# Kernel tuning notes

Hardware: AMD Instinct MI355X
Metric: run time of the kernel (lower is better)

Reference implementation:

```python
import jax, jax.numpy as jnp
import numpy as np


def setup_inputs() -> dict:
    key = jax.random.key(0)
    x = jax.random.normal(key, (16, 2048, 512), dtype=jnp.float32)
    return {"x": x}


def reference(x):
    # Cosine (L2-normalized) self-attention.
    # norm: [B, N, 1] L2 norm over feature dim
    norm = jnp.sqrt(jnp.sum(x * x, axis=2, keepdims=True))
    # scores[b, i, j] = <x_i, x_j> / (|x_i| |x_j|)  -> [B, N, N]
    scores = jnp.einsum('bnd,bmd->bnm', x, x) / (norm * jnp.swapaxes(norm, -2, -1))
    p_attn = jax.nn.softmax(scores, axis=-1)
    # output: [B, N, D]
    return jnp.einsum('bnm,bmd->bnd', p_attn, x)
```

## Files before the change

kernel.cpp:

```cpp
#include <hip/hip_runtime.h>
#include <hip/hip_bf16.h>
#include <cstdint>
#include <cstddef>

#define BB 16
#define NN 2048
#define DD 512

typedef _Float16 f16x8 __attribute__((ext_vector_type(8)));
typedef _Float16 f16x4 __attribute__((ext_vector_type(4)));
typedef float f32x4 __attribute__((ext_vector_type(4)));
typedef unsigned int u32x4 __attribute__((ext_vector_type(4)));

__device__ __forceinline__ void async_ld16(void* lds, const void* g) {
    __builtin_amdgcn_global_load_lds(
        (const __attribute__((address_space(1))) unsigned int*)(uintptr_t)g,
        (__attribute__((address_space(3))) unsigned int*)(uint32_t)(uintptr_t)lds,
        16, 0, 0);
}

#define VM_WAIT(n) asm volatile("s_waitcnt vmcnt(" #n ")" ::: "memory")
#define RAW_BAR()  do { asm volatile("" ::: "memory"); __builtin_amdgcn_s_barrier(); asm volatile("" ::: "memory"); } while (0)
#define LGKM_BAR() do { asm volatile("s_waitcnt lgkmcnt(0)" ::: "memory"); \
                        __builtin_amdgcn_s_barrier();                      \
                        __builtin_amdgcn_sched_barrier(0); } while (0)

__global__ __launch_bounds__(256) void k_prep(const float* __restrict__ x,
                                              _Float16* __restrict__ xhn,
                                              _Float16* __restrict__ vT,
                                              float* __restrict__ denom) {
    __shared__ _Float16 t[512 * 66];
    const int tid = threadIdx.x, lane = tid & 63, w = tid >> 6;
    const int b = blockIdx.y, j0 = blockIdx.x * 64;
    if (tid < 64) denom[b * NN + j0 + tid] = 0.f;
    const float* xb = x + ((size_t)b * NN + j0) * DD;

    for (int rr = 0; rr < 16; ++rr) {
        const int jj = w * 16 + rr;
        const float* xr = xb + (size_t)jj * DD;
        f32x4 a = __builtin_nontemporal_load((const f32x4*)xr + lane);
        f32x4 c = __builtin_nontemporal_load((const f32x4*)xr + lane + 64);
        float ss = a[0]*a[0] + a[1]*a[1] + a[2]*a[2] + a[3]*a[3]
                 + c[0]*c[0] + c[1]*c[1] + c[2]*c[2] + c[3]*c[3];
        #pragma unroll
        for (int o = 1; o < 64; o <<= 1) ss += __shfl_xor(ss, o);
        const float rn = 1.0f / sqrtf(ss);
        _Float16* dst = xhn + ((size_t)b * NN + j0 + jj) * DD;
        f16x4 v0 = {(_Float16)(a[0]*rn), (_Float16)(a[1]*rn), (_Float16)(a[2]*rn), (_Float16)(a[3]*rn)};
        f16x4 v1 = {(_Float16)(c[0]*rn), (_Float16)(c[1]*rn), (_Float16)(c[2]*rn), (_Float16)(c[3]*rn)};
        *(f16x4*)(dst + 4 * lane) = v0;
        *(f16x4*)(dst + 256 + 4 * lane) = v1;
        const int d0 = 4 * lane, d1 = 256 + 4 * lane;
        t[(d0 + 0) * 66 + jj] = (_Float16)a[0];
        t[(d0 + 1) * 66 + jj] = (_Float16)a[1];
        t[(d0 + 2) * 66 + jj] = (_Float16)a[2];
        t[(d0 + 3) * 66 + jj] = (_Float16)a[3];
        t[(d1 + 0) * 66 + jj] = (_Float16)c[0];
        t[(d1 + 1) * 66 + jj] = (_Float16)c[1];
        t[(d1 + 2) * 66 + jj] = (_Float16)c[2];
        t[(d1 + 3) * 66 + jj] = (_Float16)c[3];
    }
    LGKM_BAR();
    #pragma unroll
    for (int it = 0; it < 16; ++it) {
        const int id = it * 256 + tid;
        const int d = id >> 3, ch = (id & 7) * 8;
        const uint32_t* tp = (const uint32_t*)&t[d * 66 + ch];
        uint4 v = {tp[0], tp[1], tp[2], tp[3]};
        *(uint4*)(vT + ((size_t)b * DD + d) * NN + j0 + ch) = v;
    }
}

__global__ __launch_bounds__(256, 4) void k_scores(const _Float16* __restrict__ xhn,
                                                   _Float16* __restrict__ W,
                                                   float* __restrict__ denom) {
    __shared__ _Float16 smem[17408];
    const int tid = threadIdx.x;
    const int lane = tid & 63, wv = tid >> 6;
    const int wr = wv >> 1, wc = wv & 1;
    const int m_ = lane & 15, quad = lane >> 4;
    const int b = blockIdx.z;

    const int swz = (blockIdx.x % 8) * 17 + blockIdx.x / 8;
    int rem = swz, ti = 0, rowlen = NN / 128;
    while (rem >= rowlen) { rem -= rowlen; ++ti; --rowlen; }
    const int tj = ti + rem;
    const int I = ti * 128, J = tj * 128;
    const bool diag = (ti == tj);

    const _Float16* Ab = xhn + ((size_t)b * NN + I) * DD;
    const _Float16* Bb = xhn + ((size_t)b * NN + J) * DD;

    f32x4 acc[4][4];
    #pragma unroll
    for (int i = 0; i < 4; ++i)
        #pragma unroll
        for (int j = 0; j < 4; ++j) acc[i][j] = (f32x4){0.f, 0.f, 0.f, 0.f};

    const int sub = lane >> 3;
    const int swc = (lane & 7) ^ sub;
    const _Float16* agl = Ab + (size_t)(wv * 32 + sub) * DD + swc * 8;
    const _Float16* bgl = Bb + (size_t)(wv * 32 + sub) * DD + swc * 8;
    _Float16* As = smem;
    _Float16* Bs = smem + 8192;

    for (int kb = 0; kb < DD / 64; ++kb) {
        const int k0 = kb * 64;
        #pragma unroll
        for (int c = 0; c < 4; ++c) {
            async_ld16(&As[(wv * 32 + c * 8) * 64], agl + (size_t)c * 8 * DD + k0);
            async_ld16(&Bs[(wv * 32 + c * 8) * 64], bgl + (size_t)c * 8 * DD + k0);
        }
        VM_WAIT(0);
        RAW_BAR();
        __builtin_amdgcn_s_setprio(1);
        #pragma unroll
        for (int kc = 0; kc < 2; ++kc) {
            f16x8 af[4], bf[4];
            #pragma unroll
            for (int t = 0; t < 4; ++t) {
                const int Ra = wr * 64 + t * 16 + m_;
                const int Rb = wc * 64 + t * 16 + m_;
                af[t] = *(const f16x8*)&As[Ra * 64 + (((kc * 4 + quad) ^ (Ra & 7)) * 8)];
                bf[t] = *(const f16x8*)&Bs[Rb * 64 + (((kc * 4 + quad) ^ (Rb & 7)) * 8)];
            }
            #pragma unroll
            for (int i = 0; i < 4; ++i)
                #pragma unroll
                for (int j = 0; j < 4; ++j)
                    acc[i][j] = __builtin_amdgcn_mfma_f32_16x16x32_f16(af[i], bf[j], acc[i][j], 0, 0, 0);
        }
        __builtin_amdgcn_s_setprio(0);
        RAW_BAR();
    }

    f16x4 wq[4][4];
    float rowpart[4][4];
    float colpart[4] = {0.f, 0.f, 0.f, 0.f};
    #pragma unroll
    for (int i = 0; i < 4; ++i)
        #pragma unroll
        for (int r = 0; r < 4; ++r) rowpart[i][r] = 0.f;

    #pragma unroll
    for (int i = 0; i < 4; ++i) {
        #pragma unroll
        for (int j = 0; j < 4; ++j) {
            #pragma unroll
            for (int r = 0; r < 4; ++r) {
                const float w = __expf(acc[i][j][r]);
                wq[i][j][r] = (_Float16)w;
                rowpart[i][r] += w;
                colpart[j] += w;
            }
        }
    }

    #pragma unroll
    for (int i = 0; i < 4; ++i) {
        #pragma unroll
        for (int r = 0; r < 4; ++r) {
            float s = rowpart[i][r];
            s += __shfl_xor(s, 1);
            s += __shfl_xor(s, 2);
            s += __shfl_xor(s, 4);
            s += __shfl_xor(s, 8);
            if (m_ == 0)
                atomicAdd(&denom[b * NN + I + wr * 64 + i * 16 + quad * 4 + r], s);
        }
    }
    if (!diag) {
        #pragma unroll
        for (int j = 0; j < 4; ++j) {
            float s = colpart[j];
            s += __shfl_xor(s, 16);
            s += __shfl_xor(s, 32);
            if (quad == 0)
                atomicAdd(&denom[b * NN + J + wc * 64 + j * 16 + m_], s);
        }
    }

    LGKM_BAR();

    _Float16* WtT = smem;
    #pragma unroll
    for (int i = 0; i < 4; ++i) {
        const int rowb = wr * 64 + i * 16 + quad * 4;
        #pragma unroll
        for (int j = 0; j < 4; ++j) {
            const int col = wc * 64 + j * 16 + m_;
            *(f16x4*)&WtT[col * 136 + rowb] = wq[i][j];
        }
    }
    LGKM_BAR();
    #pragma unroll
    for (int it2 = 0; it2 < 8; ++it2) {
        const int id = it2 * 256 + tid;
        const int rr = id >> 4, off = (id & 15) * 8;
        *(uint4*)(W + ((size_t)b * NN + J + rr) * NN + I + off) =
            *(const uint4*)&WtT[rr * 136 + off];
    }
    if (!diag) {
        LGKM_BAR();
        _Float16* Wt = smem;
        #pragma unroll
        for (int i = 0; i < 4; ++i) {
            const int rowb = wr * 64 + i * 16 + quad * 4;
            #pragma unroll
            for (int j = 0; j < 4; ++j) {
                const int col = wc * 64 + j * 16 + m_;
                #pragma unroll
                for (int r = 0; r < 4; ++r)
                    Wt[(rowb + r) * 136 + col] = wq[i][j][r];
            }
        }
        LGKM_BAR();
        #pragma unroll
        for (int it2 = 0; it2 < 8; ++it2) {
            const int id = it2 * 256 + tid;
            const int rr = id >> 4, off = (id & 15) * 8;
            *(uint4*)(W + ((size_t)b * NN + I + rr) * NN + J + off) =
                *(const uint4*)&Wt[rr * 136 + off];
        }
    }
}

__global__ __launch_bounds__(512, 4) void k_pv(const _Float16* __restrict__ W,
                                               const _Float16* __restrict__ vT,
                                               const float* __restrict__ denom,
                                               float* __restrict__ out) {
    __shared__ _Float16 smem[24576];
    __shared__ float rdI[128];
    const int tid = threadIdx.x;
    const int lane = tid & 63, w = tid >> 6;
    const int wr = w >> 2, wcol = w & 3;
    const int m_ = lane & 15, quad = lane >> 4;

    const int bx = blockIdx.x;
    const int xcd = bx & 7, slot = bx >> 3;
    const int b  = (slot >> 5) * 8 + xcd;
    const int s2 = slot & 31;
    const int I  = (s2 >> 1) * 128;
    const int D0 = (s2 & 1) * 256;

    const _Float16* Ab = W  + ((size_t)b * NN + I) * NN;
    const _Float16* Bb = vT + ((size_t)b * DD + D0) * NN;

    const int sub = lane >> 3;
    const int swc = (lane & 7) ^ sub;
    const _Float16* agl = Ab + (size_t)(w * 16 + sub) * NN + swc * 8;
    const _Float16* bgl = Bb + (size_t)(w * 32 + sub) * NN + swc * 8;
    _Float16* As = smem;
    _Float16* Bs = smem + 8192;

    f32x4 acc[4][4];
    #pragma unroll
    for (int i = 0; i < 4; ++i)
        #pragma unroll
        for (int j = 0; j < 4; ++j) acc[i][j] = (f32x4){0.f, 0.f, 0.f, 0.f};

    for (int kb = 0; kb < NN / 64; ++kb) {
        const int k0 = kb * 64;
        #pragma unroll
        for (int c = 0; c < 2; ++c)
            async_ld16(&As[(w * 16 + c * 8) * 64], agl + (size_t)c * 8 * NN + k0);
        #pragma unroll
        for (int c = 0; c < 4; ++c)
            async_ld16(&Bs[(w * 32 + c * 8) * 64], bgl + (size_t)c * 8 * NN + k0);
        VM_WAIT(0);
        RAW_BAR();
        __builtin_amdgcn_s_setprio(1);
        #pragma unroll
        for (int kc = 0; kc < 2; ++kc) {
            f16x8 af[4], bf[4];
            #pragma unroll
            for (int t = 0; t < 4; ++t) {
                const int Ra = wr * 64 + t * 16 + m_;
                const int Rb = wcol * 64 + t * 16 + m_;
                af[t] = *(const f16x8*)&As[Ra * 64 + (((kc * 4 + quad) ^ (Ra & 7)) * 8)];
                bf[t] = *(const f16x8*)&Bs[Rb * 64 + (((kc * 4 + quad) ^ (Rb & 7)) * 8)];
            }
            #pragma unroll
            for (int i = 0; i < 4; ++i)
                #pragma unroll
                for (int j = 0; j < 4; ++j)
                    acc[i][j] = __builtin_amdgcn_mfma_f32_16x16x32_f16(af[i], bf[j], acc[i][j], 0, 0, 0);
        }
        __builtin_amdgcn_s_setprio(0);
        RAW_BAR();
    }

    if (tid < 128) rdI[tid] = 1.0f / denom[b * NN + I + tid];
    LGKM_BAR();

    #pragma unroll
    for (int i = 0; i < 4; ++i) {
        const int rowb = wr * 64 + i * 16 + quad * 4;
        #pragma unroll
        for (int r = 0; r < 4; ++r) {
            const float sc = rdI[rowb + r];
            float* op = out + ((size_t)(b * NN + I + rowb + r)) * DD + D0;
            #pragma unroll
            for (int j = 0; j < 4; ++j)
                __builtin_nontemporal_store(acc[i][j][r] * sc,
                                            op + wcol * 64 + j * 16 + m_);
        }
    }
}

extern "C" void kernel_launch(void* const* d_in, const int* in_sizes, int n_in,
                              void* d_out, int out_size, void* d_ws, size_t ws_size,
                              hipStream_t stream) {
    const float* x = (const float*)d_in[0];
    char* ws = (char*)d_ws;
    _Float16* xhn   = (_Float16*)(ws);
    _Float16* vT    = (_Float16*)(ws + (size_t)33554432);
    _Float16* W     = (_Float16*)(ws + (size_t)67108864);
    float*    denom = (float*)   (ws + (size_t)201326592);
    float*    out   = (float*)d_out;

    k_prep<<<dim3(NN / 64, BB), 256, 0, stream>>>(x, xhn, vT, denom);
    const int npairs = (NN / 128) * (NN / 128 + 1) / 2;
    k_scores<<<dim3(npairs, 1, BB), 256, 0, stream>>>(xhn, W, denom);
    k_pv<<<dim3(512, 1, 1), 512, 0, stream>>>(W, vT, denom, out);
}
```

Before: 175.4 us.

## Enlarge PV tile to 256x256 with double-buffered async loads and interleaved MFMA

The PV GEMM kernel now computes a 256-row by 256-column output tile per block, so half as many blocks launch (256). It double-buffers 64-wide K tiles in dynamic LDS (about 129 KB) and prefetches two stages ahead. The MFMA work is split into quarters, with LDS fragment reads and the next global prefetch interleaved between them. The aim is to raise data reuse per block and hide global-load latency behind compute, in place of the previous load, wait and compute loop. In exchange each block holds twice the accumulators, occupancy drops, and there are more barriers per K step.

```diff
diff --git a/kernel.cpp b/kernel.cpp
--- a/kernel.cpp
+++ b/kernel.cpp
@@ -24,6 +24,8 @@
 #define LGKM_BAR() do { asm volatile("s_waitcnt lgkmcnt(0)" ::: "memory"); \
                         __builtin_amdgcn_s_barrier();                      \
                         __builtin_amdgcn_sched_barrier(0); } while (0)
+#define LGKM0_FENCE() do { asm volatile("s_waitcnt lgkmcnt(0)" ::: "memory"); \
+                           __builtin_amdgcn_sched_barrier(0); } while (0)
 
 __global__ __launch_bounds__(256) void k_prep(const float* __restrict__ x,
                                               _Float16* __restrict__ xhn,
@@ -225,12 +227,12 @@
     }
 }
 
-__global__ __launch_bounds__(512, 4) void k_pv(const _Float16* __restrict__ W,
+__global__ __launch_bounds__(512, 2) void k_pv(const _Float16* __restrict__ W,
                                                const _Float16* __restrict__ vT,
                                                const float* __restrict__ denom,
                                                float* __restrict__ out) {
-    __shared__ _Float16 smem[24576];
-    __shared__ float rdI[128];
+    extern __shared__ _Float16 smem[];
+    float* rdI = (float*)(smem + 65536);
     const int tid = threadIdx.x;
     const int lane = tid & 63, w = tid >> 6;
     const int wr = w >> 2, wcol = w & 3;
@@ -238,64 +240,103 @@
 
     const int bx = blockIdx.x;
     const int xcd = bx & 7, slot = bx >> 3;
-    const int b  = (slot >> 5) * 8 + xcd;
-    const int s2 = slot & 31;
-    const int I  = (s2 >> 1) * 128;
+    const int b  = (slot >> 4) * 8 + xcd;
+    const int s2 = slot & 15;
+    const int I  = (s2 >> 1) * 256;
     const int D0 = (s2 & 1) * 256;
 
     const _Float16* Ab = W  + ((size_t)b * NN + I) * NN;
     const _Float16* Bb = vT + ((size_t)b * DD + D0) * NN;
 
-    const int sub = lane >> 3;
-    const int swc = (lane & 7) ^ sub;
-    const _Float16* agl = Ab + (size_t)(w * 16 + sub) * NN + swc * 8;
-    const _Float16* bgl = Bb + (size_t)(w * 32 + sub) * NN + swc * 8;
-    _Float16* As = smem;
-    _Float16* Bs = smem + 8192;
-
-    f32x4 acc[4][4];
-    #pragma unroll
-    for (int i = 0; i < 4; ++i)
+    const int srow = tid >> 3;
+    const int scol = ((tid & 7) ^ (srow & 7)) * 8;
+    const _Float16* aglb = Ab + (size_t)srow * NN + scol;
+    const _Float16* bglb = Bb + (size_t)srow * NN + scol;
+
+    f32x4 acc[8][4];
+    #pragma unroll
+    for (int i = 0; i < 8; ++i)
         #pragma unroll
         for (int j = 0; j < 4; ++j) acc[i][j] = (f32x4){0.f, 0.f, 0.f, 0.f};
 
-    for (int kb = 0; kb < NN / 64; ++kb) {
-        const int k0 = kb * 64;
-        #pragma unroll
-        for (int c = 0; c < 2; ++c)
-            async_ld16(&As[(w * 16 + c * 8) * 64], agl + (size_t)c * 8 * NN + k0);
-        #pragma unroll
-        for (int c = 0; c < 4; ++c)
-            async_ld16(&Bs[(w * 32 + c * 8) * 64], bgl + (size_t)c * 8 * NN + k0);
-        VM_WAIT(0);
-        RAW_BAR();
-        __builtin_amdgcn_s_setprio(1);
-        #pragma unroll
-        for (int kc = 0; kc < 2; ++kc) {
-            f16x8 af[4], bf[4];
-            #pragma unroll
-            for (int t = 0; t < 4; ++t) {
-                const int Ra = wr * 64 + t * 16 + m_;
-                const int Rb = wcol * 64 + t * 16 + m_;
-                af[t] = *(const f16x8*)&As[Ra * 64 + (((kc * 4 + quad) ^ (Ra & 7)) * 8)];
-                bf[t] = *(const f16x8*)&Bs[Rb * 64 + (((kc * 4 + quad) ^ (Rb & 7)) * 8)];
-            }
-            #pragma unroll
-            for (int i = 0; i < 4; ++i)
-                #pragma unroll
-                for (int j = 0; j < 4; ++j)
-                    acc[i][j] = __builtin_amdgcn_mfma_f32_16x16x32_f16(af[i], bf[j], acc[i][j], 0, 0, 0);
-        }
-        __builtin_amdgcn_s_setprio(0);
-        RAW_BAR();
-    }
-
-    if (tid < 128) rdI[tid] = 1.0f / denom[b * NN + I + tid];
+#define STG(t_, l_)                                                            \
+    async_ld16(&smem[((t_) & 1) * 32768 + ((l_) & 1) * 16384 +                 \
+                     ((l_) >> 1) * 4096 + w * 512],                            \
+               ((l_) & 1 ? bglb : aglb) + (size_t)((l_) >> 1) * 64 * NN +      \
+                   (t_) * 64)
+
+#define PV_LDA(dst_, i8_) do {                                                 \
+    const int Ra = wr * 128 + (i8_) * 16 + m_;                                 \
+    _Pragma("unroll")                                                          \
+    for (int kc = 0; kc < 2; ++kc)                                             \
+        dst_[kc] = *(const f16x8*)&smem[cur * 32768 + Ra * 64 +                \
+                                        (((kc * 4 + quad) ^ (Ra & 7)) * 8)];   \
+    } while (0)
+
+#define PV_MFMA(q_, A0_, A1_) do {                                             \
+    __builtin_amdgcn_s_setprio(1);                                             \
+    _Pragma("unroll")                                                          \
+    for (int jt = 0; jt < 4; ++jt)                                             \
+        _Pragma("unroll")                                                      \
+        for (int kc = 0; kc < 2; ++kc) {                                       \
+            acc[(q_)*2+0][jt] = __builtin_amdgcn_mfma_f32_16x16x32_f16(        \
+                A0_[kc], bf[jt][kc], acc[(q_)*2+0][jt], 0, 0, 0);              \
+            acc[(q_)*2+1][jt] = __builtin_amdgcn_mfma_f32_16x16x32_f16(        \
+                A1_[kc], bf[jt][kc], acc[(q_)*2+1][jt], 0, 0, 0);              \
+        }                                                                      \
+    __builtin_amdgcn_s_setprio(0);                                             \
+    } while (0)
+
+    #pragma unroll
+    for (int l = 0; l < 8; ++l) STG(0, l);
+    #pragma unroll
+    for (int l = 0; l < 8; ++l) STG(1, l);
+
+    const int NT = NN / 64;
+    for (int tc = 0; tc < NT; ++tc) {
+        const int cur = tc & 1;
+        if (tc == NT - 1) { VM_WAIT(0); } else { VM_WAIT(8); }
+        RAW_BAR();
+        f16x8 bf[4][2], afA[2][2], afB[2][2];
+        #pragma unroll
+        for (int jt = 0; jt < 4; ++jt) {
+            const int Rb = wcol * 64 + jt * 16 + m_;
+            #pragma unroll
+            for (int kc = 0; kc < 2; ++kc)
+                bf[jt][kc] = *(const f16x8*)&smem[cur * 32768 + 16384 + Rb * 64 +
+                                                  (((kc * 4 + quad) ^ (Rb & 7)) * 8)];
+        }
+        PV_LDA(afA[0], 0); PV_LDA(afA[1], 1);
+        RAW_BAR();
+        LGKM0_FENCE();
+        PV_MFMA(0, afA[0], afA[1]);
+        RAW_BAR();
+        PV_LDA(afB[0], 2); PV_LDA(afB[1], 3);
+        RAW_BAR();
+        LGKM0_FENCE();
+        PV_MFMA(1, afB[0], afB[1]);
+        RAW_BAR();
+        PV_LDA(afA[0], 4); PV_LDA(afA[1], 5);
+        PV_LDA(afB[0], 6); PV_LDA(afB[1], 7);
+        RAW_BAR();
+        LGKM0_FENCE();
+        PV_MFMA(2, afA[0], afA[1]);
+        RAW_BAR();
+        if (tc + 2 < NT) {
+            #pragma unroll
+            for (int l = 0; l < 8; ++l) STG(tc + 2, l);
+        }
+        RAW_BAR();
+        PV_MFMA(3, afB[0], afB[1]);
+        RAW_BAR();
+    }
+
+    if (tid < 256) rdI[tid] = 1.0f / denom[b * NN + I + tid];
     LGKM_BAR();
 
     #pragma unroll
-    for (int i = 0; i < 4; ++i) {
-        const int rowb = wr * 64 + i * 16 + quad * 4;
+    for (int i = 0; i < 8; ++i) {
+        const int rowb = wr * 128 + i * 16 + quad * 4;
         #pragma unroll
         for (int r = 0; r < 4; ++r) {
             const float sc = rdI[rowb + r];
@@ -306,6 +347,9 @@
                                             op + wcol * 64 + j * 16 + m_);
         }
     }
+#undef STG
+#undef PV_LDA
+#undef PV_MFMA
 }
 
 extern "C" void kernel_launch(void* const* d_in, const int* in_sizes, int n_in,
@@ -322,5 +366,5 @@
     k_prep<<<dim3(NN / 64, BB), 256, 0, stream>>>(x, xhn, vT, denom);
     const int npairs = (NN / 128) * (NN / 128 + 1) / 2;
     k_scores<<<dim3(npairs, 1, BB), 256, 0, stream>>>(xhn, W, denom);
-    k_pv<<<dim3(512, 1, 1), 512, 0, stream>>>(W, vT, denom, out);
-}
+    k_pv<<<dim3(256, 1, 1), 512, 132096, stream>>>(W, vT, denom, out);
+}
```

Measured after the change: 185.8 us. 1.06x slower.
